# Kernel tuning notes

Measured on AMD Instinct MI355X. Metric: run time of the kernel, lower is better.

## Reference

```python
import jax, jax.numpy as jnp
import numpy as np

N_NODES = 100000
N_EDGES = 1600000
IN_CH, HID_CH, OUT_CH = 128, 64, 40


def setup_inputs() -> dict:
    key = jax.random.key(0)
    k_x, k_e, k_w1, k_w2 = jax.random.split(key, 4)
    x = jax.random.normal(k_x, (N_NODES, IN_CH), dtype=jnp.float32)
    edge_index = jax.random.randint(k_e, (2, N_EDGES), 0, N_NODES, dtype=jnp.int64)
    # Glorot-ish scaled weights, zero bias (matches GCNConv init convention)
    W1 = jax.random.normal(k_w1, (IN_CH, HID_CH), dtype=jnp.float32) / np.sqrt(IN_CH)
    b1 = jnp.zeros((HID_CH,), dtype=jnp.float32)
    W2 = jax.random.normal(k_w2, (HID_CH, OUT_CH), dtype=jnp.float32) / np.sqrt(HID_CH)
    b2 = jnp.zeros((OUT_CH,), dtype=jnp.float32)
    return {"x": x, "edge_index": edge_index, "W1": W1, "b1": b1, "W2": W2, "b2": b2}


def _gcn_conv(x, edge_index, W, b, n):
    """GCNConv with normalize=True: linear transform, add self-loops,
    symmetric D^-1/2 A D^-1/2 aggregation (source_to_target flow), bias."""
    h = x @ W  # [n, out]
    loops = jnp.arange(n, dtype=edge_index.dtype)
    row = jnp.concatenate([edge_index[0], loops])  # sources
    col = jnp.concatenate([edge_index[1], loops])  # targets
    deg = jax.ops.segment_sum(jnp.ones_like(col, dtype=h.dtype), col, num_segments=n)
    dinv = jnp.where(deg > 0, jax.lax.rsqrt(deg), jnp.zeros_like(deg))
    w = dinv[row] * dinv[col]  # [E+n] per-edge norm
    out = jax.ops.segment_sum(h[row] * w[:, None], col, num_segments=n)  # scatter-add to targets
    return out + b


def reference(x, edge_index, W1, b1, W2, b2):
    # eval mode: F.dropout(p=0.8, training=False) is identity
    n = x.shape[0]
    h = jax.nn.relu(_gcn_conv(x, edge_index, W1, b1, n))
    return _gcn_conv(h, edge_index, W2, b2, n)  # [N, OUT_CH] logits
```

## Files before the change

kernel.cpp:

```cpp
#include <hip/hip_runtime.h>

#define N_NODES 100000
#define N_EDGES 1600000
#define IN_CH   128
#define HID_CH  64
#define OUT_CH  40
#define NBKT    196
#define EPB     4096
#define CAP     9216
#define NWIN    16
#define WPITCH  17

using bf16x8 = __attribute__((ext_vector_type(8))) short;
using f32x4  = __attribute__((ext_vector_type(4))) float;

__device__ __forceinline__ float bf2f(unsigned short u) {
    union { unsigned int i; float f; } c; c.i = ((unsigned int)u) << 16; return c.f;
}
__device__ __forceinline__ unsigned short f2bf(float f) {
    union { float f; unsigned int i; } c; c.f = f;
    unsigned int r = c.i + 0x7FFFu + ((c.i >> 16) & 1u);
    return (unsigned short)(r >> 16);
}
__device__ __forceinline__ float4 bf2f4(ushort4 u) {
    return make_float4(bf2f(u.x), bf2f(u.y), bf2f(u.z), bf2f(u.w));
}

__global__ void k_bin(const int* __restrict__ ei, int* __restrict__ gcur,
                      int* __restrict__ ebuf) {
    __shared__ int hist[NBKT];
    __shared__ int lcur[NBKT];
    int tid = threadIdx.x;
    int base = blockIdx.x * EPB;
    int nloc = N_EDGES - base;
    if (nloc > EPB) nloc = EPB;
    int n4 = nloc >> 2;
    const int4* S4 = (const int4*)(ei + base);
    const int4* D4 = (const int4*)(ei + N_EDGES + base);

    if (tid < NBKT) { hist[tid] = 0; }
    __syncthreads();
    for (int i = tid; i < n4; i += 256) {
        int4 d = D4[i];
        atomicAdd(&hist[d.x >> 9], 1);
        atomicAdd(&hist[d.y >> 9], 1);
        atomicAdd(&hist[d.z >> 9], 1);
        atomicAdd(&hist[d.w >> 9], 1);
    }
    __syncthreads();
    if (tid < NBKT) {
        int h = hist[tid];
        lcur[tid] = h ? (tid * CAP + atomicAdd(&gcur[tid], h)) : 0;
    }
    __syncthreads();
    for (int i = tid; i < n4; i += 256) {
        int4 s = S4[i];
        int4 d = D4[i];
        int p;
        p = atomicAdd(&lcur[d.x >> 9], 1); ebuf[p] = s.x | ((d.x & 511) << 17);
        p = atomicAdd(&lcur[d.y >> 9], 1); ebuf[p] = s.y | ((d.y & 511) << 17);
        p = atomicAdd(&lcur[d.z >> 9], 1); ebuf[p] = s.z | ((d.z & 511) << 17);
        p = atomicAdd(&lcur[d.w >> 9], 1); ebuf[p] = s.w | ((d.w & 511) << 17);
    }
}

__global__ void k_node(const int* __restrict__ gcur, const int* __restrict__ ebuf,
                       int* __restrict__ row_start, int* __restrict__ row_end,
                       int* __restrict__ csr_src, float* __restrict__ dinv) {
    __shared__ int cnt2[512 * WPITCH];
    __shared__ int s[512];
    int tid = threadIdx.x;
    int b = blockIdx.x;
    int node0 = b << 9;
    int lo = b * CAP;
    int hi = lo + gcur[b];
    int n = hi - lo, n4 = n >> 2;
    const int4* E4 = (const int4*)(ebuf + lo);

#define BIN_OF(w) (((unsigned)(w) >> 17) * WPITCH + (((w) & 0x1FFFF) >> 13))

    for (int i = tid; i < 512 * WPITCH; i += 512) cnt2[i] = 0;
    __syncthreads();
    for (int i = tid; i < n4; i += 512) {
        int4 w = E4[i];
        atomicAdd(&cnt2[BIN_OF(w.x)], 1);
        atomicAdd(&cnt2[BIN_OF(w.y)], 1);
        atomicAdd(&cnt2[BIN_OF(w.z)], 1);
        atomicAdd(&cnt2[BIN_OF(w.w)], 1);
    }
    for (int e = lo + (n4 << 2) + tid; e < hi; e += 512)
        atomicAdd(&cnt2[BIN_OF(ebuf[e])], 1);
    __syncthreads();

    int tmp[NWIN];
    int c = 0;
#pragma unroll
    for (int w = 0; w < NWIN; ++w) {
        tmp[w] = c;
        c += cnt2[tid * WPITCH + w];
    }
    s[tid] = c;
    __syncthreads();
#pragma unroll
    for (int off = 1; off < 512; off <<= 1) {
        int tv = (tid >= off) ? s[tid - off] : 0;
        __syncthreads();
        s[tid] += tv;
        __syncthreads();
    }
    int nodestart = lo + s[tid] - c;
    int node = node0 + tid;
    if (node < N_NODES) {
        row_start[node] = nodestart;
        row_end[node]   = nodestart + c;
        dinv[node] = rsqrtf(1.0f + (float)c);
    }
#pragma unroll
    for (int w = 0; w < NWIN; ++w)
        cnt2[tid * WPITCH + w] = nodestart + tmp[w];
    __syncthreads();

    for (int i = tid; i < n4; i += 512) {
        int4 w = E4[i];
        int p;
        p = atomicAdd(&cnt2[BIN_OF(w.x)], 1); csr_src[p] = w.x & 0x1FFFF;
        p = atomicAdd(&cnt2[BIN_OF(w.y)], 1); csr_src[p] = w.y & 0x1FFFF;
        p = atomicAdd(&cnt2[BIN_OF(w.z)], 1); csr_src[p] = w.z & 0x1FFFF;
        p = atomicAdd(&cnt2[BIN_OF(w.w)], 1); csr_src[p] = w.w & 0x1FFFF;
    }
    for (int e = lo + (n4 << 2) + tid; e < hi; e += 512) {
        int w = ebuf[e];
        int p = atomicAdd(&cnt2[BIN_OF(w)], 1);
        csr_src[p] = w & 0x1FFFF;
    }
#undef BIN_OF
}

__global__ __launch_bounds__(256, 4)
void k_gemm1(const float* __restrict__ x, const float* __restrict__ W1,
             const float* __restrict__ dinv, unsigned short* __restrict__ h1s) {
    __shared__ unsigned short Al[64 * 136];
    __shared__ unsigned short Bl[64 * 136];
    __shared__ float dl[64];
    int tid = threadIdx.x;
    long long node0 = (long long)blockIdx.x * 64;

    const float4* X = (const float4*)x;
    for (int i = tid; i < 64 * 32; i += 256) {
        int r = i >> 5, c4 = i & 31;
        long long gr = node0 + r;
        if (gr >= N_NODES) gr = N_NODES - 1;
        float4 v = X[gr * 32 + c4];
        *(ushort4*)&Al[r * 136 + c4 * 4] =
            make_ushort4(f2bf(v.x), f2bf(v.y), f2bf(v.z), f2bf(v.w));
    }
    for (int i = tid; i < 128 * 64; i += 256) {
        int k = i >> 6, nn = i & 63;
        Bl[nn * 136 + k] = f2bf(W1[i]);
    }
    if (tid < 64) {
        long long gr = node0 + tid;
        dl[tid] = dinv[gr < N_NODES ? gr : N_NODES - 1];
    }
    __syncthreads();

    int lane = tid & 63, wave = tid >> 6;
    int quad = lane >> 4, l16 = lane & 15;
    int arow = wave * 16 + l16;
    f32x4 ac0 = {0,0,0,0}, ac1 = {0,0,0,0}, ac2 = {0,0,0,0}, ac3 = {0,0,0,0};

#pragma unroll
    for (int ks = 0; ks < 4; ++ks) {
        int ko = ks * 32 + quad * 8;
        bf16x8 a  = *(const bf16x8*)&Al[arow * 136 + ko];
        bf16x8 b0 = *(const bf16x8*)&Bl[( 0 + l16) * 136 + ko];
        bf16x8 b1 = *(const bf16x8*)&Bl[(16 + l16) * 136 + ko];
        bf16x8 b2 = *(const bf16x8*)&Bl[(32 + l16) * 136 + ko];
        bf16x8 b3 = *(const bf16x8*)&Bl[(48 + l16) * 136 + ko];
        ac0 = __builtin_amdgcn_mfma_f32_16x16x32_bf16(a, b0, ac0, 0, 0, 0);
        ac1 = __builtin_amdgcn_mfma_f32_16x16x32_bf16(a, b1, ac1, 0, 0, 0);
        ac2 = __builtin_amdgcn_mfma_f32_16x16x32_bf16(a, b2, ac2, 0, 0, 0);
        ac3 = __builtin_amdgcn_mfma_f32_16x16x32_bf16(a, b3, ac3, 0, 0, 0);
    }

#pragma unroll
    for (int r = 0; r < 4; ++r) {
        int rl = wave * 16 + quad * 4 + r;
        long long grow = node0 + rl;
        if (grow < N_NODES) {
            float dd = dl[rl];
            h1s[grow * 64 +  0 + l16] = f2bf(ac0[r] * dd);
            h1s[grow * 64 + 16 + l16] = f2bf(ac1[r] * dd);
            h1s[grow * 64 + 32 + l16] = f2bf(ac2[r] * dd);
            h1s[grow * 64 + 48 + l16] = f2bf(ac3[r] * dd);
        }
    }
}

__global__ __launch_bounds__(256, 4)
void k_agg1g2(const int* __restrict__ row_start, const int* __restrict__ row_end,
              const int* __restrict__ csr_src,
              const unsigned short* __restrict__ h1s, const float* __restrict__ dinv,
              const float* __restrict__ b1, const float* __restrict__ W2,
              unsigned short* __restrict__ h2s) {
    __shared__ unsigned short Al[64 * 72];
    __shared__ unsigned short Bl[48 * 72];
    __shared__ float dl[64];
    int tid = threadIdx.x;
    long long node0 = (long long)blockIdx.x * 64;

    for (int i = tid; i < 48 * 64; i += 256) {
        int nn = i >> 6, k = i & 63;
        Bl[nn * 72 + k] = f2bf(nn < OUT_CH ? W2[k * OUT_CH + nn] : 0.0f);
    }
    if (tid < 64) {
        long long gr = node0 + tid;
        dl[tid] = dinv[gr < N_NODES ? gr : N_NODES - 1];
    }
    __syncthreads();

    int cg = tid & 15;
    int nsub = tid >> 4;
    float4 bb = ((const float4*)b1)[cg];
    const ushort4* H = (const ushort4*)h1s;

#pragma unroll
    for (int r4 = 0; r4 < 4; ++r4) {
        int nl = r4 * 16 + nsub;
        long long node = node0 + nl;
        ushort4 res = make_ushort4(0, 0, 0, 0);
        if (node < N_NODES) {
            int e = row_start[node];
            int f = row_end[node];
            float4 acc = bf2f4(H[node * 16 + cg]);
            float4 acc2 = {0.f, 0.f, 0.f, 0.f};
            while (f - e >= 8) {
                int s0 = csr_src[e];
                int s1 = csr_src[e + 1];
                int s2 = csr_src[e + 2];
                int s3 = csr_src[e + 3];
                int s4 = csr_src[e + 4];
                int s5 = csr_src[e + 5];
                int s6 = csr_src[e + 6];
                int s7 = csr_src[e + 7];
                float4 v0 = bf2f4(H[(long long)s0 * 16 + cg]);
                float4 v1 = bf2f4(H[(long long)s1 * 16 + cg]);
                float4 v2 = bf2f4(H[(long long)s2 * 16 + cg]);
                float4 v3 = bf2f4(H[(long long)s3 * 16 + cg]);
                float4 u0 = bf2f4(H[(long long)s4 * 16 + cg]);
                float4 u1 = bf2f4(H[(long long)s5 * 16 + cg]);
                float4 u2 = bf2f4(H[(long long)s6 * 16 + cg]);
                float4 u3 = bf2f4(H[(long long)s7 * 16 + cg]);
                acc.x  += (v0.x + v1.x) + (v2.x + v3.x);
                acc.y  += (v0.y + v1.y) + (v2.y + v3.y);
                acc.z  += (v0.z + v1.z) + (v2.z + v3.z);
                acc.w  += (v0.w + v1.w) + (v2.w + v3.w);
                acc2.x += (u0.x + u1.x) + (u2.x + u3.x);
                acc2.y += (u0.y + u1.y) + (u2.y + u3.y);
                acc2.z += (u0.z + u1.z) + (u2.z + u3.z);
                acc2.w += (u0.w + u1.w) + (u2.w + u3.w);
                e += 8;
            }
            for (; e < f; ++e) {
                float4 v = bf2f4(H[(long long)csr_src[e] * 16 + cg]);
                acc.x += v.x; acc.y += v.y; acc.z += v.z; acc.w += v.w;
            }
            acc.x += acc2.x; acc.y += acc2.y; acc.z += acc2.z; acc.w += acc2.w;
            float dd = dl[nl];
            res = make_ushort4(f2bf(fmaxf(acc.x * dd + bb.x, 0.f)),
                               f2bf(fmaxf(acc.y * dd + bb.y, 0.f)),
                               f2bf(fmaxf(acc.z * dd + bb.z, 0.f)),
                               f2bf(fmaxf(acc.w * dd + bb.w, 0.f)));
        }
        *(ushort4*)&Al[nl * 72 + cg * 4] = res;
    }
    __syncthreads();

    int lane = tid & 63, wave = tid >> 6;
    int quad = lane >> 4, l16 = lane & 15;
    int arow = wave * 16 + l16;
    f32x4 ac0 = {0,0,0,0}, ac1 = {0,0,0,0}, ac2 = {0,0,0,0};

#pragma unroll
    for (int ks = 0; ks < 2; ++ks) {
        int ko = ks * 32 + quad * 8;
        bf16x8 a  = *(const bf16x8*)&Al[arow * 72 + ko];
        bf16x8 b0 = *(const bf16x8*)&Bl[( 0 + l16) * 72 + ko];
        bf16x8 b1v = *(const bf16x8*)&Bl[(16 + l16) * 72 + ko];
        bf16x8 b2 = *(const bf16x8*)&Bl[(32 + l16) * 72 + ko];
        ac0 = __builtin_amdgcn_mfma_f32_16x16x32_bf16(a, b0, ac0, 0, 0, 0);
        ac1 = __builtin_amdgcn_mfma_f32_16x16x32_bf16(a, b1v, ac1, 0, 0, 0);
        ac2 = __builtin_amdgcn_mfma_f32_16x16x32_bf16(a, b2, ac2, 0, 0, 0);
    }

#pragma unroll
    for (int r = 0; r < 4; ++r) {
        int rl = wave * 16 + quad * 4 + r;
        long long grow = node0 + rl;
        if (grow < N_NODES) {
            float dd = dl[rl];
            h2s[grow * 40 +  0 + l16] = f2bf(ac0[r] * dd);
            h2s[grow * 40 + 16 + l16] = f2bf(ac1[r] * dd);
            if (l16 < 8) h2s[grow * 40 + 32 + l16] = f2bf(ac2[r] * dd);
        }
    }
}

__global__ void k_agg2(const int* __restrict__ row_start, const int* __restrict__ row_end,
                       const int* __restrict__ csr_src,
                       const unsigned short* __restrict__ h2s, const float* __restrict__ dinv,
                       const float* __restrict__ b2, float* __restrict__ out) {
    int idx = blockIdx.x * blockDim.x + threadIdx.x;
    int node = idx >> 4;
    int cg = idx & 15;
    if (node >= N_NODES || cg >= 10) return;
    int e = row_start[node];
    int f = row_end[node];
    const ushort4* H = (const ushort4*)h2s;
    float4 acc = bf2f4(H[(long long)node * 10 + cg]);
    float4 acc2 = {0.f, 0.f, 0.f, 0.f};
    while (f - e >= 8) {
        int s0 = csr_src[e];
        int s1 = csr_src[e + 1];
        int s2 = csr_src[e + 2];
        int s3 = csr_src[e + 3];
        int s4 = csr_src[e + 4];
        int s5 = csr_src[e + 5];
        int s6 = csr_src[e + 6];
        int s7 = csr_src[e + 7];
        float4 v0 = bf2f4(H[(long long)s0 * 10 + cg]);
        float4 v1 = bf2f4(H[(long long)s1 * 10 + cg]);
        float4 v2 = bf2f4(H[(long long)s2 * 10 + cg]);
        float4 v3 = bf2f4(H[(long long)s3 * 10 + cg]);
        float4 u0 = bf2f4(H[(long long)s4 * 10 + cg]);
        float4 u1 = bf2f4(H[(long long)s5 * 10 + cg]);
        float4 u2 = bf2f4(H[(long long)s6 * 10 + cg]);
        float4 u3 = bf2f4(H[(long long)s7 * 10 + cg]);
        acc.x  += (v0.x + v1.x) + (v2.x + v3.x);
        acc.y  += (v0.y + v1.y) + (v2.y + v3.y);
        acc.z  += (v0.z + v1.z) + (v2.z + v3.z);
        acc.w  += (v0.w + v1.w) + (v2.w + v3.w);
        acc2.x += (u0.x + u1.x) + (u2.x + u3.x);
        acc2.y += (u0.y + u1.y) + (u2.y + u3.y);
        acc2.z += (u0.z + u1.z) + (u2.z + u3.z);
        acc2.w += (u0.w + u1.w) + (u2.w + u3.w);
        e += 8;
    }
    for (; e < f; ++e) {
        float4 v = bf2f4(H[(long long)csr_src[e] * 10 + cg]);
        acc.x += v.x; acc.y += v.y; acc.z += v.z; acc.w += v.w;
    }
    acc.x += acc2.x; acc.y += acc2.y; acc.z += acc2.z; acc.w += acc2.w;
    float dd = dinv[node];
    float4 b = ((const float4*)b2)[cg];
    acc.x = acc.x * dd + b.x;
    acc.y = acc.y * dd + b.y;
    acc.z = acc.z * dd + b.z;
    acc.w = acc.w * dd + b.w;
    ((float4*)out)[(long long)node * 10 + cg] = acc;
}

extern "C" void kernel_launch(void* const* d_in, const int* in_sizes, int n_in,
                              void* d_out, int out_size, void* d_ws, size_t ws_size,
                              hipStream_t stream) {
    const float* x  = (const float*)d_in[0];
    const int*   ei = (const int*)d_in[1];
    const float* W1 = (const float*)d_in[2];
    const float* b1 = (const float*)d_in[3];
    const float* W2 = (const float*)d_in[4];
    const float* b2 = (const float*)d_in[5];
    float* out = (float*)d_out;

    unsigned short* hbuf  = (unsigned short*)d_ws;
    unsigned short* h2buf = hbuf + 64LL * N_NODES;
    int* ebuf      = (int*)(h2buf + 64LL * N_NODES);
    int* csr_src   = ebuf + NBKT * CAP;
    int* row_start = csr_src + NBKT * CAP;
    int* row_end   = row_start + N_NODES;
    int* gcur      = row_end + N_NODES;
    float* dinv    = (float*)(gcur + 256);

    const int B = 256;
    const int g16 = (N_NODES * 16 + B - 1) / B;
    const int gRows = (N_NODES + 63) / 64;

    hipMemsetAsync((void*)gcur, 0, NBKT * sizeof(int), stream);
    k_bin<<<(N_EDGES + EPB - 1) / EPB, B, 0, stream>>>(ei, gcur, ebuf);
    k_node<<<NBKT, 512, 0, stream>>>(gcur, ebuf, row_start, row_end, csr_src, dinv);

    k_gemm1<<<gRows, B, 0, stream>>>(x, W1, dinv, hbuf);
    k_agg1g2<<<gRows, B, 0, stream>>>(row_start, row_end, csr_src, hbuf, dinv,
                                      b1, W2, h2buf);
    k_agg2<<<g16, B, 0, stream>>>(row_start, row_end, csr_src, h2buf, dinv, b2, out);
}
```

Baseline: 225.1 us.

## Pad CSR rows to multiples of eight with dummy zero node, drop tail loops

Each node's CSR segment is padded to a multiple of 8 entries filled with a dummy source index pointing at a zeroed padding row of h1/h2. This lets both aggregation kernels drop their scalar tail loops. The k_node pass also drops the sub-window bucketing that ordered sources within a row, so source locality in the gathers is lost. k_agg1g2 now handles 32 nodes per block with a higher occupancy hint, and only two waves run the MFMA. The cost is extra gathers of the zero row and more CSR memory.

```diff
diff --git a/kernel.cpp b/kernel.cpp
--- a/kernel.cpp
+++ b/kernel.cpp
@@ -1,6 +1,7 @@
 #include <hip/hip_runtime.h>
 
 #define N_NODES 100000
+#define NPAD    100032
 #define N_EDGES 1600000
 #define IN_CH   128
 #define HID_CH  64
@@ -8,8 +9,7 @@
 #define NBKT    196
 #define EPB     4096
 #define CAP     9216
-#define NWIN    16
-#define WPITCH  17
+#define CAPC    10752
 
 using bf16x8 = __attribute__((ext_vector_type(8))) short;
 using f32x4  = __attribute__((ext_vector_type(4))) float;
@@ -67,39 +67,32 @@
 __global__ void k_node(const int* __restrict__ gcur, const int* __restrict__ ebuf,
                        int* __restrict__ row_start, int* __restrict__ row_end,
                        int* __restrict__ csr_src, float* __restrict__ dinv) {
-    __shared__ int cnt2[512 * WPITCH];
+    __shared__ int cnt[512];
     __shared__ int s[512];
     int tid = threadIdx.x;
     int b = blockIdx.x;
     int node0 = b << 9;
     int lo = b * CAP;
+    int lo2 = b * CAPC;
     int hi = lo + gcur[b];
     int n = hi - lo, n4 = n >> 2;
     const int4* E4 = (const int4*)(ebuf + lo);
 
-#define BIN_OF(w) (((unsigned)(w) >> 17) * WPITCH + (((w) & 0x1FFFF) >> 13))
-
-    for (int i = tid; i < 512 * WPITCH; i += 512) cnt2[i] = 0;
+    cnt[tid] = 0;
     __syncthreads();
     for (int i = tid; i < n4; i += 512) {
         int4 w = E4[i];
-        atomicAdd(&cnt2[BIN_OF(w.x)], 1);
-        atomicAdd(&cnt2[BIN_OF(w.y)], 1);
-        atomicAdd(&cnt2[BIN_OF(w.z)], 1);
-        atomicAdd(&cnt2[BIN_OF(w.w)], 1);
+        atomicAdd(&cnt[(unsigned)w.x >> 17], 1);
+        atomicAdd(&cnt[(unsigned)w.y >> 17], 1);
+        atomicAdd(&cnt[(unsigned)w.z >> 17], 1);
+        atomicAdd(&cnt[(unsigned)w.w >> 17], 1);
     }
     for (int e = lo + (n4 << 2) + tid; e < hi; e += 512)
-        atomicAdd(&cnt2[BIN_OF(ebuf[e])], 1);
-    __syncthreads();
-
-    int tmp[NWIN];
-    int c = 0;
-#pragma unroll
-    for (int w = 0; w < NWIN; ++w) {
-        tmp[w] = c;
-        c += cnt2[tid * WPITCH + w];
-    }
-    s[tid] = c;
+        atomicAdd(&cnt[(unsigned)ebuf[e] >> 17], 1);
+    __syncthreads();
+    int c = cnt[tid];
+    int cp = (c + 7) & ~7;
+    s[tid] = cp;
     __syncthreads();
 #pragma unroll
     for (int off = 1; off < 512; off <<= 1) {
@@ -108,32 +101,31 @@
         s[tid] += tv;
         __syncthreads();
     }
-    int nodestart = lo + s[tid] - c;
+    int nodestart = lo2 + s[tid] - cp;
     int node = node0 + tid;
     if (node < N_NODES) {
         row_start[node] = nodestart;
         row_end[node]   = nodestart + c;
         dinv[node] = rsqrtf(1.0f + (float)c);
     }
-#pragma unroll
-    for (int w = 0; w < NWIN; ++w)
-        cnt2[tid * WPITCH + w] = nodestart + tmp[w];
-    __syncthreads();
-
+    __syncthreads();
+    cnt[tid] = nodestart;
+    __syncthreads();
     for (int i = tid; i < n4; i += 512) {
         int4 w = E4[i];
         int p;
-        p = atomicAdd(&cnt2[BIN_OF(w.x)], 1); csr_src[p] = w.x & 0x1FFFF;
-        p = atomicAdd(&cnt2[BIN_OF(w.y)], 1); csr_src[p] = w.y & 0x1FFFF;
-        p = atomicAdd(&cnt2[BIN_OF(w.z)], 1); csr_src[p] = w.z & 0x1FFFF;
-        p = atomicAdd(&cnt2[BIN_OF(w.w)], 1); csr_src[p] = w.w & 0x1FFFF;
+        p = atomicAdd(&cnt[(unsigned)w.x >> 17], 1); csr_src[p] = w.x & 0x1FFFF;
+        p = atomicAdd(&cnt[(unsigned)w.y >> 17], 1); csr_src[p] = w.y & 0x1FFFF;
+        p = atomicAdd(&cnt[(unsigned)w.z >> 17], 1); csr_src[p] = w.z & 0x1FFFF;
+        p = atomicAdd(&cnt[(unsigned)w.w >> 17], 1); csr_src[p] = w.w & 0x1FFFF;
     }
     for (int e = lo + (n4 << 2) + tid; e < hi; e += 512) {
         int w = ebuf[e];
-        int p = atomicAdd(&cnt2[BIN_OF(w)], 1);
+        int p = atomicAdd(&cnt[(unsigned)w >> 17], 1);
         csr_src[p] = w & 0x1FFFF;
     }
-#undef BIN_OF
+    for (int p = nodestart + c; p < nodestart + cp; ++p)
+        csr_src[p] = N_NODES;
 }
 
 __global__ __launch_bounds__(256, 4)
@@ -193,27 +185,32 @@
             h1s[grow * 64 + 16 + l16] = f2bf(ac1[r] * dd);
             h1s[grow * 64 + 32 + l16] = f2bf(ac2[r] * dd);
             h1s[grow * 64 + 48 + l16] = f2bf(ac3[r] * dd);
+        } else {
+            h1s[grow * 64 +  0 + l16] = 0;
+            h1s[grow * 64 + 16 + l16] = 0;
+            h1s[grow * 64 + 32 + l16] = 0;
+            h1s[grow * 64 + 48 + l16] = 0;
         }
     }
 }
 
-__global__ __launch_bounds__(256, 4)
+__global__ __launch_bounds__(256, 8)
 void k_agg1g2(const int* __restrict__ row_start, const int* __restrict__ row_end,
               const int* __restrict__ csr_src,
               const unsigned short* __restrict__ h1s, const float* __restrict__ dinv,
               const float* __restrict__ b1, const float* __restrict__ W2,
               unsigned short* __restrict__ h2s) {
-    __shared__ unsigned short Al[64 * 72];
+    __shared__ unsigned short Al[32 * 72];
     __shared__ unsigned short Bl[48 * 72];
-    __shared__ float dl[64];
+    __shared__ float dl[32];
     int tid = threadIdx.x;
-    long long node0 = (long long)blockIdx.x * 64;
+    long long node0 = (long long)blockIdx.x * 32;
 
     for (int i = tid; i < 48 * 64; i += 256) {
         int nn = i >> 6, k = i & 63;
         Bl[nn * 72 + k] = f2bf(nn < OUT_CH ? W2[k * OUT_CH + nn] : 0.0f);
     }
-    if (tid < 64) {
+    if (tid < 32) {
         long long gr = node0 + tid;
         dl[tid] = dinv[gr < N_NODES ? gr : N_NODES - 1];
     }
@@ -225,16 +222,17 @@
     const ushort4* H = (const ushort4*)h1s;
 
 #pragma unroll
-    for (int r4 = 0; r4 < 4; ++r4) {
+    for (int r4 = 0; r4 < 2; ++r4) {
         int nl = r4 * 16 + nsub;
         long long node = node0 + nl;
         ushort4 res = make_ushort4(0, 0, 0, 0);
         if (node < N_NODES) {
             int e = row_start[node];
             int f = row_end[node];
+            int f8 = e + ((f - e + 7) & ~7);
             float4 acc = bf2f4(H[node * 16 + cg]);
             float4 acc2 = {0.f, 0.f, 0.f, 0.f};
-            while (f - e >= 8) {
+            while (e < f8) {
                 int s0 = csr_src[e];
                 int s1 = csr_src[e + 1];
                 int s2 = csr_src[e + 2];
@@ -261,10 +259,6 @@
                 acc2.w += (u0.w + u1.w) + (u2.w + u3.w);
                 e += 8;
             }
-            for (; e < f; ++e) {
-                float4 v = bf2f4(H[(long long)csr_src[e] * 16 + cg]);
-                acc.x += v.x; acc.y += v.y; acc.z += v.z; acc.w += v.w;
-            }
             acc.x += acc2.x; acc.y += acc2.y; acc.z += acc2.z; acc.w += acc2.w;
             float dd = dl[nl];
             res = make_ushort4(f2bf(fmaxf(acc.x * dd + bb.x, 0.f)),
@@ -277,31 +271,37 @@
     __syncthreads();
 
     int lane = tid & 63, wave = tid >> 6;
-    int quad = lane >> 4, l16 = lane & 15;
-    int arow = wave * 16 + l16;
-    f32x4 ac0 = {0,0,0,0}, ac1 = {0,0,0,0}, ac2 = {0,0,0,0};
-
-#pragma unroll
-    for (int ks = 0; ks < 2; ++ks) {
-        int ko = ks * 32 + quad * 8;
-        bf16x8 a  = *(const bf16x8*)&Al[arow * 72 + ko];
-        bf16x8 b0 = *(const bf16x8*)&Bl[( 0 + l16) * 72 + ko];
-        bf16x8 b1v = *(const bf16x8*)&Bl[(16 + l16) * 72 + ko];
-        bf16x8 b2 = *(const bf16x8*)&Bl[(32 + l16) * 72 + ko];
-        ac0 = __builtin_amdgcn_mfma_f32_16x16x32_bf16(a, b0, ac0, 0, 0, 0);
-        ac1 = __builtin_amdgcn_mfma_f32_16x16x32_bf16(a, b1v, ac1, 0, 0, 0);
-        ac2 = __builtin_amdgcn_mfma_f32_16x16x32_bf16(a, b2, ac2, 0, 0, 0);
-    }
-
-#pragma unroll
-    for (int r = 0; r < 4; ++r) {
-        int rl = wave * 16 + quad * 4 + r;
-        long long grow = node0 + rl;
-        if (grow < N_NODES) {
-            float dd = dl[rl];
-            h2s[grow * 40 +  0 + l16] = f2bf(ac0[r] * dd);
-            h2s[grow * 40 + 16 + l16] = f2bf(ac1[r] * dd);
-            if (l16 < 8) h2s[grow * 40 + 32 + l16] = f2bf(ac2[r] * dd);
+    if (wave < 2) {
+        int quad = lane >> 4, l16 = lane & 15;
+        int arow = wave * 16 + l16;
+        f32x4 ac0 = {0,0,0,0}, ac1 = {0,0,0,0}, ac2 = {0,0,0,0};
+
+#pragma unroll
+        for (int ks = 0; ks < 2; ++ks) {
+            int ko = ks * 32 + quad * 8;
+            bf16x8 a  = *(const bf16x8*)&Al[arow * 72 + ko];
+            bf16x8 b0 = *(const bf16x8*)&Bl[( 0 + l16) * 72 + ko];
+            bf16x8 b1v = *(const bf16x8*)&Bl[(16 + l16) * 72 + ko];
+            bf16x8 b2 = *(const bf16x8*)&Bl[(32 + l16) * 72 + ko];
+            ac0 = __builtin_amdgcn_mfma_f32_16x16x32_bf16(a, b0, ac0, 0, 0, 0);
+            ac1 = __builtin_amdgcn_mfma_f32_16x16x32_bf16(a, b1v, ac1, 0, 0, 0);
+            ac2 = __builtin_amdgcn_mfma_f32_16x16x32_bf16(a, b2, ac2, 0, 0, 0);
+        }
+
+#pragma unroll
+        for (int r = 0; r < 4; ++r) {
+            int rl = wave * 16 + quad * 4 + r;
+            long long grow = node0 + rl;
+            if (grow < N_NODES) {
+                float dd = dl[rl];
+                h2s[grow * 40 +  0 + l16] = f2bf(ac0[r] * dd);
+                h2s[grow * 40 + 16 + l16] = f2bf(ac1[r] * dd);
+                if (l16 < 8) h2s[grow * 40 + 32 + l16] = f2bf(ac2[r] * dd);
+            } else if (grow < NPAD) {
+                h2s[grow * 40 +  0 + l16] = 0;
+                h2s[grow * 40 + 16 + l16] = 0;
+                if (l16 < 8) h2s[grow * 40 + 32 + l16] = 0;
+            }
         }
     }
 }
@@ -316,10 +316,11 @@
     if (node >= N_NODES || cg >= 10) return;
     int e = row_start[node];
     int f = row_end[node];
+    int f8 = e + ((f - e + 7) & ~7);
     const ushort4* H = (const ushort4*)h2s;
     float4 acc = bf2f4(H[(long long)node * 10 + cg]);
     float4 acc2 = {0.f, 0.f, 0.f, 0.f};
-    while (f - e >= 8) {
+    while (e < f8) {
         int s0 = csr_src[e];
         int s1 = csr_src[e + 1];
         int s2 = csr_src[e + 2];
@@ -346,10 +347,6 @@
         acc2.w += (u0.w + u1.w) + (u2.w + u3.w);
         e += 8;
     }
-    for (; e < f; ++e) {
-        float4 v = bf2f4(H[(long long)csr_src[e] * 10 + cg]);
-        acc.x += v.x; acc.y += v.y; acc.z += v.z; acc.w += v.w;
-    }
     acc.x += acc2.x; acc.y += acc2.y; acc.z += acc2.z; acc.w += acc2.w;
     float dd = dinv[node];
     float4 b = ((const float4*)b2)[cg];
@@ -372,24 +369,25 @@
     float* out = (float*)d_out;
 
     unsigned short* hbuf  = (unsigned short*)d_ws;
-    unsigned short* h2buf = hbuf + 64LL * N_NODES;
-    int* ebuf      = (int*)(h2buf + 64LL * N_NODES);
+    unsigned short* h2buf = hbuf + 64LL * NPAD;
+    int* ebuf      = (int*)(h2buf + 40LL * NPAD);
     int* csr_src   = ebuf + NBKT * CAP;
-    int* row_start = csr_src + NBKT * CAP;
+    int* row_start = csr_src + NBKT * CAPC;
     int* row_end   = row_start + N_NODES;
     int* gcur      = row_end + N_NODES;
     float* dinv    = (float*)(gcur + 256);
 
     const int B = 256;
     const int g16 = (N_NODES * 16 + B - 1) / B;
-    const int gRows = (N_NODES + 63) / 64;
+    const int gRows = NPAD / 64;
+    const int gAgg  = NPAD / 32;
 
     hipMemsetAsync((void*)gcur, 0, NBKT * sizeof(int), stream);
     k_bin<<<(N_EDGES + EPB - 1) / EPB, B, 0, stream>>>(ei, gcur, ebuf);
     k_node<<<NBKT, 512, 0, stream>>>(gcur, ebuf, row_start, row_end, csr_src, dinv);
 
     k_gemm1<<<gRows, B, 0, stream>>>(x, W1, dinv, hbuf);
-    k_agg1g2<<<gRows, B, 0, stream>>>(row_start, row_end, csr_src, hbuf, dinv,
-                                      b1, W2, h2buf);
+    k_agg1g2<<<gAgg, B, 0, stream>>>(row_start, row_end, csr_src, hbuf, dinv,
+                                     b1, W2, h2buf);
     k_agg2<<<g16, B, 0, stream>>>(row_start, row_end, csr_src, h2buf, dinv, b2, out);
 }
```

Result: faster. 220.4 us (-2.1%).
